# Kernel tuning notes

Hardware: AMD Instinct MI355X
Metric: run time of the kernel (lower is better)

The kernel has to match this reference:

```python
import jax, jax.numpy as jnp
import numpy as np

VOCAB = 50257
FEATURES = 128
RESERVOIR = 8
FROZEN_INDEX = 0
B, S = 16, 2048


def setup_inputs() -> dict:
    key = jax.random.key(0)
    k1, k2, k3 = jax.random.split(key, 3)
    base_indices = jax.random.randint(k1, (B, S), 0, VOCAB, dtype=jnp.int64 if jax.config.jax_enable_x64 else jnp.int32)
    reservoir_lookup = jax.random.randint(k2, (VOCAB, RESERVOIR), 0, VOCAB, dtype=jnp.int64 if jax.config.jax_enable_x64 else jnp.int32)
    embedding_weight = jax.random.normal(k3, (VOCAB, FEATURES), dtype=jnp.float32)
    return {"base_indices": base_indices, "reservoir_lookup": reservoir_lookup, "embedding_weight": embedding_weight}


def reference(base_indices, reservoir_lookup, embedding_weight):
    # Zero out the frozen row (value and, via the mask, its gradient --
    # equivalent to the straight-through masking in the torch module).
    vocab = embedding_weight.shape[0]
    mask = (jnp.arange(vocab) != FROZEN_INDEX).astype(embedding_weight.dtype)[:, None]  # [V,1]
    w_eff = embedding_weight * mask                       # [V,F], frozen row = 0
    reservoir_indices = reservoir_lookup[base_indices]    # [B,S,R]
    gathered = w_eff[reservoir_indices]                   # [B,S,R,F]
    return jnp.sum(gathered, axis=-2)                     # [B,S,F]
```

## Files before the change

### kernel.cpp

```cpp
#include <hip/hip_runtime.h>


#define VOCAB 50257
#define FEATURES 128
#define RESERVOIR 8
#define NTOK (16 * 2048)

typedef float float4v __attribute__((ext_vector_type(4)));

__global__ __launch_bounds__(256) void reservoir_embed_kernel(
    const int* __restrict__ base_indices,
    const int* __restrict__ reservoir_lookup,
    const float* __restrict__ weight,
    float* __restrict__ out)
{
    const int gid  = blockIdx.x * blockDim.x + threadIdx.x;
    const int tok  = gid >> 5;
    const int lane = gid & 31;

    const int base = base_indices[tok];
    const int4* rlp = reinterpret_cast<const int4*>(reservoir_lookup + base * RESERVOIR);
    const int4 i0 = rlp[0];
    const int4 i1 = rlp[1];
    const int idx[RESERVOIR] = {i0.x, i0.y, i0.z, i0.w, i1.x, i1.y, i1.z, i1.w};

    float4v rows[RESERVOIR];
#pragma unroll
    for (int r = 0; r < RESERVOIR; ++r) {
        const float* p = weight + (((unsigned)idx[r]) << 7) + (lane << 2);
        asm volatile("global_load_dwordx4 %0, %1, off sc0"
                     : "=v"(rows[r]) : "v"(p));
    }
    asm volatile("s_waitcnt vmcnt(0)"
                 : "+v"(rows[0]), "+v"(rows[1]), "+v"(rows[2]), "+v"(rows[3]),
                   "+v"(rows[4]), "+v"(rows[5]), "+v"(rows[6]), "+v"(rows[7]));

    float4v acc = {0.f, 0.f, 0.f, 0.f};
#pragma unroll
    for (int r = 0; r < RESERVOIR; ++r) {
        const float m = (idx[r] != 0) ? 1.0f : 0.0f;
        acc += m * rows[r];
    }

    float4v* op = reinterpret_cast<float4v*>(out + (unsigned)tok * FEATURES + (lane << 2));
    __builtin_nontemporal_store(acc, op);
}

extern "C" void kernel_launch(void* const* d_in, const int* in_sizes, int n_in,
                              void* d_out, int out_size, void* d_ws, size_t ws_size,
                              hipStream_t stream) {
    (void)in_sizes; (void)n_in; (void)out_size; (void)d_ws; (void)ws_size;
    const int*   base_indices     = (const int*)d_in[0];
    const int*   reservoir_lookup = (const int*)d_in[1];
    const float* weight           = (const float*)d_in[2];
    float*       out              = (float*)d_out;

    const int threads = 256;
    const int total   = NTOK * 32;
    const int blocks  = total / threads;
    reservoir_embed_kernel<<<blocks, threads, 0, stream>>>(
        base_indices, reservoir_lookup, weight, out);
}
```

Before: 25.34 us.

## Process four tokens per 32-lane group with plain loads instead of inline asm

Each 32-lane group now handles four consecutive tokens. It loads their base indices with one int4 load and fetches all four reservoir index rows before gathering the embedding rows. The hand-written global_load with sc0 and explicit waitcnt is replaced by ordinary vector loads, so the compiler schedules the waits and no longer uses the sc0 cache hint. The grid shrinks by a factor of four in exchange for more memory-level parallelism per thread, at the cost of higher register pressure and less occupancy.

```diff
diff --git a/kernel.cpp b/kernel.cpp
--- a/kernel.cpp
+++ b/kernel.cpp
@@ -5,6 +5,7 @@
 #define FEATURES 128
 #define RESERVOIR 8
 #define NTOK (16 * 2048)
+#define TPG 4
 
 typedef float float4v __attribute__((ext_vector_type(4)));
 
@@ -15,35 +16,49 @@
     float* __restrict__ out)
 {
     const int gid  = blockIdx.x * blockDim.x + threadIdx.x;
-    const int tok  = gid >> 5;
+    const int grp  = gid >> 5;
     const int lane = gid & 31;
+    const int t0   = grp * TPG;
 
-    const int base = base_indices[tok];
-    const int4* rlp = reinterpret_cast<const int4*>(reservoir_lookup + base * RESERVOIR);
-    const int4 i0 = rlp[0];
-    const int4 i1 = rlp[1];
-    const int idx[RESERVOIR] = {i0.x, i0.y, i0.z, i0.w, i1.x, i1.y, i1.z, i1.w};
+    const int4 b4 = *reinterpret_cast<const int4*>(base_indices + t0);
+    const int bases[TPG] = {b4.x, b4.y, b4.z, b4.w};
 
-    float4v rows[RESERVOIR];
+    int idx[TPG][RESERVOIR];
 #pragma unroll
-    for (int r = 0; r < RESERVOIR; ++r) {
-        const float* p = weight + (((unsigned)idx[r]) << 7) + (lane << 2);
-        asm volatile("global_load_dwordx4 %0, %1, off sc0"
-                     : "=v"(rows[r]) : "v"(p));
-    }
-    asm volatile("s_waitcnt vmcnt(0)"
-                 : "+v"(rows[0]), "+v"(rows[1]), "+v"(rows[2]), "+v"(rows[3]),
-                   "+v"(rows[4]), "+v"(rows[5]), "+v"(rows[6]), "+v"(rows[7]));
-
-    float4v acc = {0.f, 0.f, 0.f, 0.f};
-#pragma unroll
-    for (int r = 0; r < RESERVOIR; ++r) {
-        const float m = (idx[r] != 0) ? 1.0f : 0.0f;
-        acc += m * rows[r];
+    for (int t = 0; t < TPG; ++t) {
+        const int4* rlp = reinterpret_cast<const int4*>(
+            reservoir_lookup + bases[t] * RESERVOIR);
+        const int4 i0 = rlp[0];
+        const int4 i1 = rlp[1];
+        idx[t][0] = i0.x; idx[t][1] = i0.y; idx[t][2] = i0.z; idx[t][3] = i0.w;
+        idx[t][4] = i1.x; idx[t][5] = i1.y; idx[t][6] = i1.z; idx[t][7] = i1.w;
     }
 
-    float4v* op = reinterpret_cast<float4v*>(out + (unsigned)tok * FEATURES + (lane << 2));
-    __builtin_nontemporal_store(acc, op);
+    float4v acc[TPG];
+#pragma unroll
+    for (int t = 0; t < TPG; ++t) acc[t] = (float4v){0.f, 0.f, 0.f, 0.f};
+
+#pragma unroll
+    for (int t = 0; t < TPG; ++t) {
+        float4v rows[RESERVOIR];
+#pragma unroll
+        for (int r = 0; r < RESERVOIR; ++r) {
+            rows[r] = *reinterpret_cast<const float4v*>(
+                weight + (((unsigned)idx[t][r]) << 7) + (lane << 2));
+        }
+#pragma unroll
+        for (int r = 0; r < RESERVOIR; ++r) {
+            const float m = (idx[t][r] != 0) ? 1.0f : 0.0f;
+            acc[t] += m * rows[r];
+        }
+    }
+
+#pragma unroll
+    for (int t = 0; t < TPG; ++t) {
+        float4v* op = reinterpret_cast<float4v*>(
+            out + (unsigned)(t0 + t) * FEATURES + (lane << 2));
+        __builtin_nontemporal_store(acc[t], op);
+    }
 }
 
 extern "C" void kernel_launch(void* const* d_in, const int* in_sizes, int n_in,
@@ -56,8 +71,8 @@
     float*       out              = (float*)d_out;
 
     const int threads = 256;
-    const int total   = NTOK * 32;
-    const int blocks  = total / threads;
+    const int groups  = NTOK / TPG;
+    const int blocks  = groups * 32 / threads;
     reservoir_embed_kernel<<<blocks, threads, 0, stream>>>(
         base_indices, reservoir_lookup, weight, out);
 }
```

Result: no change. 24.86 us (-1.9%).

## Split feature dimension into slices across blocks with multi-pass token loops

Applied to the files above, without the earlier changes.

Each block now handles one 16-feature slice for 256 tokens over four passes, with four threads per token, instead of 32 threads covering all 128 features of one token. Neighbouring blocks take different slices of the same tokens, so each slice's gathered weight rows (64 bytes per row) are meant to stay in a smaller cache working set. The cost is that every token's lookup indices are read eight times, once per slice, and each wave's stores become scattered 64-byte pieces. The inline-asm loads with sc0 and the explicit waitcnt are replaced by plain loads, and launch bounds now request four blocks per CU.

```diff
diff --git a/kernel.cpp b/kernel.cpp
--- a/kernel.cpp
+++ b/kernel.cpp
@@ -5,45 +5,56 @@
 #define FEATURES 128
 #define RESERVOIR 8
 #define NTOK (16 * 2048)
+#define NSLICE 8
+#define SLICE_F 16
+#define TOK_PER_BLOCK 256
+#define PASSES 4
 
 typedef float float4v __attribute__((ext_vector_type(4)));
 
-__global__ __launch_bounds__(256) void reservoir_embed_kernel(
+__global__ __launch_bounds__(256, 4) void reservoir_embed_kernel(
     const int* __restrict__ base_indices,
     const int* __restrict__ reservoir_lookup,
     const float* __restrict__ weight,
     float* __restrict__ out)
 {
-    const int gid  = blockIdx.x * blockDim.x + threadIdx.x;
-    const int tok  = gid >> 5;
-    const int lane = gid & 31;
+    const int tid   = threadIdx.x;
+    const int slice = blockIdx.x & (NSLICE - 1);
+    const int chunk = blockIdx.x >> 3;
+    const int c     = tid & 3;
+    const int fbase = slice * SLICE_F + c * 4;
 
-    const int base = base_indices[tok];
-    const int4* rlp = reinterpret_cast<const int4*>(reservoir_lookup + base * RESERVOIR);
-    const int4 i0 = rlp[0];
-    const int4 i1 = rlp[1];
-    const int idx[RESERVOIR] = {i0.x, i0.y, i0.z, i0.w, i1.x, i1.y, i1.z, i1.w};
+    const int tok0 = chunk * TOK_PER_BLOCK;
 
-    float4v rows[RESERVOIR];
+#pragma unroll 2
+    for (int p = 0; p < PASSES; ++p) {
+        const int tok = tok0 + p * 64 + (tid >> 2);
+
+        const int base = base_indices[tok];
+        const int4* rlp = reinterpret_cast<const int4*>(
+            reservoir_lookup + base * RESERVOIR);
+        const int4 i0 = rlp[0];
+        const int4 i1 = rlp[1];
+        const int idx[RESERVOIR] = {i0.x, i0.y, i0.z, i0.w, i1.x, i1.y, i1.z, i1.w};
+
+        float4v rows[RESERVOIR];
 #pragma unroll
-    for (int r = 0; r < RESERVOIR; ++r) {
-        const float* p = weight + (((unsigned)idx[r]) << 7) + (lane << 2);
-        asm volatile("global_load_dwordx4 %0, %1, off sc0"
-                     : "=v"(rows[r]) : "v"(p));
+        for (int r = 0; r < RESERVOIR; ++r) {
+            rows[r] = *reinterpret_cast<const float4v*>(
+                weight + (((unsigned)idx[r]) << 7) + fbase);
+        }
+
+        float4v acc = {0.f, 0.f, 0.f, 0.f};
+#pragma unroll
+        for (int r = 0; r < RESERVOIR; ++r) {
+            const float m = (idx[r] != 0) ? 1.0f : 0.0f;
+            acc += m * rows[r];
+        }
+
+        float4v* op = reinterpret_cast<float4v*>(
+            out + (unsigned)tok * FEATURES + fbase);
+        __builtin_nontemporal_store(acc, op);
     }
-    asm volatile("s_waitcnt vmcnt(0)"
-                 : "+v"(rows[0]), "+v"(rows[1]), "+v"(rows[2]), "+v"(rows[3]),
-                   "+v"(rows[4]), "+v"(rows[5]), "+v"(rows[6]), "+v"(rows[7]));
-
-    float4v acc = {0.f, 0.f, 0.f, 0.f};
-#pragma unroll
-    for (int r = 0; r < RESERVOIR; ++r) {
-        const float m = (idx[r] != 0) ? 1.0f : 0.0f;
-        acc += m * rows[r];
-    }
-
-    float4v* op = reinterpret_cast<float4v*>(out + (unsigned)tok * FEATURES + (lane << 2));
-    __builtin_nontemporal_store(acc, op);
 }
 
 extern "C" void kernel_launch(void* const* d_in, const int* in_sizes, int n_in,
@@ -55,9 +66,7 @@
     const float* weight           = (const float*)d_in[2];
     float*       out              = (float*)d_out;
 
-    const int threads = 256;
-    const int total   = NTOK * 32;
-    const int blocks  = total / threads;
-    reservoir_embed_kernel<<<blocks, threads, 0, stream>>>(
+    const int blocks  = NSLICE * (NTOK / TOK_PER_BLOCK);
+    reservoir_embed_kernel<<<blocks, 256, 0, stream>>>(
         base_indices, reservoir_lookup, weight, out);
 }
```

New measurement: 28.79 us. 13.6% more time.
